# Kernel optimization log

Hardware: AMD Instinct MI355X
Metric: run time of the kernel (lower is better)

The kernel has to match this reference:

```python
import jax, jax.numpy as jnp
import numpy as np

B, S, D_IN, D_OUT = 4, 2048, 1024, 1024


def setup_inputs() -> dict:
    key = jax.random.key(0)
    k1, k2, k3, k4 = jax.random.split(key, 4)
    x = jax.random.normal(k1, (B, S, D_IN), dtype=jnp.float32)
    scale = 1.0 / np.sqrt(D_IN)
    Wq = jax.random.normal(k2, (D_IN, D_OUT), dtype=jnp.float32) * scale
    Wk = jax.random.normal(k3, (D_IN, D_OUT), dtype=jnp.float32) * scale
    Wv = jax.random.normal(k4, (D_IN, D_OUT), dtype=jnp.float32) * scale
    return {"x": x, "Wq": Wq, "Wk": Wk, "Wv": Wv}


def reference(x, Wq, Wk, Wv):
    # QKV projections (Linear, no bias)
    q = jnp.einsum('bsd,de->bse', x, Wq)  # [B,S,D_OUT]
    k = jnp.einsum('bsd,de->bse', x, Wk)
    v = jnp.einsum('bsd,de->bse', x, Wv)
    d_out = Wq.shape[1]
    # raw scores [B,S,S], scaled after masking (identical math: -inf stays -inf)
    scores = jnp.einsum('bqe,bke->bqk', q, k) * (d_out ** -0.5)
    S_ = x.shape[1]
    # causal mask: future positions (j > i) are masked out
    causal = jnp.triu(jnp.ones((S_, S_), dtype=bool), k=1)
    scores = jnp.where(causal[None, :, :], -jnp.inf, scores)
    attn = jax.nn.softmax(scores, axis=-1)  # dropout p=0.0 -> identity
    return jnp.einsum('bqk,bke->bqe', attn, v)
```

## Files before the change

### kernel.cpp

```cpp
#include <hip/hip_runtime.h>
#include <stdint.h>

typedef unsigned short u16;
typedef unsigned int u32;
typedef __bf16 bf16x8 __attribute__((ext_vector_type(8)));
typedef float f32x4 __attribute__((ext_vector_type(4)));

#define BM 128
#define BN 128
#define BK 64

__device__ __forceinline__ u16 f2bf(float x) {
  union { float f; uint32_t u; } c; c.f = x;
  uint32_t r = (c.u + 0x7FFFu + ((c.u >> 16) & 1u)) >> 16;
  return (u16)r;
}

__device__ __forceinline__ void async_copy16(const u16* g, u16* l) {
  __builtin_amdgcn_global_load_lds(
      (const __attribute__((address_space(1))) void*)g,
      (__attribute__((address_space(3))) void*)l,
      16, 0, 0);
}

__global__ void flag_init(u32* __restrict__ f) { if (threadIdx.x == 0) *f = 0; }

__global__ void detect_dtype(const u16* __restrict__ w, u32* __restrict__ cnt) {
  int i = blockIdx.x * 256 + threadIdx.x;
  if ((w[i] & 0x7F80u) == 0x7F80u) atomicAdd(cnt, 1u);
}

__global__ void normalize_all(const void* __restrict__ s0, const void* __restrict__ s1,
                              const void* __restrict__ s2, const void* __restrict__ s3,
                              u16* __restrict__ dst, const u32* __restrict__ flag,
                              long n0, long n1) {
  long i = (long)blockIdx.x * 256 + threadIdx.x;
  const void* src;
  long j;
  if (i < n0) { src = s0; j = i; }
  else {
    long t = i - n0;
    long w = t / n1;
    j = t - w * n1;
    src = (w == 0) ? s1 : (w == 1) ? s2 : s3;
  }
  if (*flag > 32) dst[i] = f2bf(((const float*)src)[j]);
  else            dst[i] = ((const u16*)src)[j];
}

__global__ void zerofill_u16(u16* __restrict__ p) {
  long i = (long)blockIdx.x * 256 + threadIdx.x;
  p[i] = 0;
}

template <int MODE>
__global__ __launch_bounds__(256, 2)
void gemm_nt(const u16* __restrict__ A, const u16* __restrict__ B, void* __restrict__ Cv,
             const u32* __restrict__ flag,
             int K, int lda, int ldb, int ldc,
             long sA, long sB, long sC, long cOff,
             float scale, int causal, int trik)
{
  const int bm = blockIdx.y, bn = blockIdx.x, bz = blockIdx.z;
  if (causal && bn > bm) return;

  __shared__ u16 As[BM * BK];
  __shared__ u16 Bs[BN * BK];

  A += (long)bz * sA;
  B += (long)bz * sB;

  const int tid  = threadIdx.x;
  const int wid  = tid >> 6;
  const int lane = tid & 63;
  const int l16  = lane & 15;
  const int lk   = lane >> 4;
  const int srow = lane >> 3;
  const int swz  = ((lane & 7) ^ srow) * 8;
  const int m0 = bm * BM, n0 = bn * BN;

  int nk = K / BK;
  if (trik) { int lim = (m0 + BM) / BK; if (lim < nk) nk = lim; }

  f32x4 acc[4][4] = {};

  for (int kt = 0; kt < nk; ++kt) {
    const int k0 = kt * BK;
#pragma unroll
    for (int c = 0; c < 4; ++c) {
      const int rb = wid * 32 + c * 8;
      async_copy16(A + (long)(m0 + rb + srow) * lda + (k0 + swz), As + rb * BK);
      async_copy16(B + (long)(n0 + rb + srow) * ldb + (k0 + swz), Bs + rb * BK);
    }
    __syncthreads();
#pragma unroll
    for (int kh = 0; kh < 2; ++kh) {
      bf16x8 av[4], bv[4];
#pragma unroll
      for (int i = 0; i < 4; ++i) {
        const int Ra = (wid >> 1) * 64 + i * 16 + l16;
        const int Rb = (wid & 1)  * 64 + i * 16 + l16;
        const int ca = ((kh * 4 + lk) ^ (l16 & 7)) * 8;
        av[i] = *(const bf16x8*)(As + Ra * BK + ca);
        bv[i] = *(const bf16x8*)(Bs + Rb * BK + ca);
      }
#pragma unroll
      for (int mi = 0; mi < 4; ++mi)
#pragma unroll
        for (int ni = 0; ni < 4; ++ni)
          acc[mi][ni] = __builtin_amdgcn_mfma_f32_16x16x32_bf16(av[mi], bv[ni], acc[mi][ni], 0, 0, 0);
    }
    __syncthreads();
  }

  const int rb0 = m0 + (wid >> 1) * 64;
  const int cb0 = n0 + (wid & 1) * 64;
  const long cbase = (long)bz * sC + cOff;
  const bool f32out = (MODE == 1) || (MODE == 2 && *flag > 32);

#pragma unroll
  for (int mi = 0; mi < 4; ++mi)
#pragma unroll
    for (int ni = 0; ni < 4; ++ni) {
      const int row = rb0 + mi * 16 + lk * 4;
      const int col = cb0 + ni * 16 + l16;
#pragma unroll
      for (int r = 0; r < 4; ++r) {
        const float v = acc[mi][ni][r] * scale;
        const long idx = cbase + (long)(row + r) * ldc + col;
        if constexpr (MODE == 0) {
          ((u16*)Cv)[idx] = f2bf(v);
        } else if constexpr (MODE == 1) {
          ((float*)Cv)[idx] = v;
        } else {
          if (f32out) ((float*)Cv)[idx] = v;
          else        ((u16*)Cv)[idx]   = f2bf(v);
        }
      }
    }
}

__global__ __launch_bounds__(256)
void transpose_bf16(const u16* __restrict__ in, u16* __restrict__ out,
                    int ldIn, int ldOut, long sIn, long sOut)
{
  __shared__ u16 tile[64][72];
  const int bz = blockIdx.z;
  in  += (long)bz * sIn;
  out += (long)bz * sOut;
  const int r0 = blockIdx.y * 64, c0 = blockIdx.x * 64;
  const int tid = threadIdx.x;
#pragma unroll
  for (int p = 0; p < 2; ++p) {
    int v = tid + p * 256;
    int row = v >> 3, c8 = (v & 7) * 8;
    union { uint4 q; u16 s[8]; } t;
    t.q = *(const uint4*)(in + (long)(r0 + row) * ldIn + c0 + c8);
#pragma unroll
    for (int i = 0; i < 8; ++i) tile[row][c8 + i] = t.s[i];
  }
  __syncthreads();
#pragma unroll
  for (int p = 0; p < 2; ++p) {
    int v = tid + p * 256;
    int oc = v >> 3, r8 = (v & 7) * 8;
    union { uint4 q; u16 s[8]; } t;
#pragma unroll
    for (int i = 0; i < 8; ++i) t.s[i] = tile[r8 + i][oc];
    *(uint4*)(out + (long)(c0 + oc) * ldOut + r0 + r8) = t.q;
  }
}

__global__ __launch_bounds__(256)
void softmax_causal(char* __restrict__ base, long rowStrideB, int S, int modS)
{
  const long r = blockIdx.x;
  const int i = (int)(r % modS);
  float* sc = (float*)(base + r * rowStrideB);
  u16*   pr = (u16*)(base + r * rowStrideB);
  const int n = i + 1;
  const int tid = threadIdx.x;
  const int wv = tid >> 6, lane = tid & 63;
  __shared__ float red[4];

  float e[8];
  int cnt = 0;
  float m = -3.0e38f;
  for (int j = tid; j < n; j += 256) { float x = sc[j]; e[cnt++] = x; m = fmaxf(m, x); }
#pragma unroll
  for (int o = 32; o > 0; o >>= 1) m = fmaxf(m, __shfl_xor(m, o));
  if (lane == 0) red[wv] = m;
  __syncthreads();
  m = fmaxf(fmaxf(red[0], red[1]), fmaxf(red[2], red[3]));
  __syncthreads();

  float s = 0.f;
#pragma unroll
  for (int c = 0; c < 8; ++c)
    if (c < cnt) { float x = __expf(e[c] - m); e[c] = x; s += x; }
#pragma unroll
  for (int o = 32; o > 0; o >>= 1) s += __shfl_xor(s, o);
  if (lane == 0) red[wv] = s;
  __syncthreads();
  s = red[0] + red[1] + red[2] + red[3];
  const float inv = 1.0f / s;

  cnt = 0;
  for (int j = tid; j < S; j += 256) {
    u16 v = 0;
    if (j < n) v = f2bf(e[cnt++] * inv);
    pr[j] = v;
  }
}

extern "C" void kernel_launch(void* const* d_in, const int* in_sizes, int n_in,
                              void* d_out, int out_size, void* d_ws, size_t ws_size,
                              hipStream_t stream)
{
  (void)in_sizes; (void)n_in; (void)out_size;
  const int Bb = 4, S = 2048, D = 1024, D3 = 3072;
  const long SD = (long)S * D;
  const long SS = (long)S * S;
  const long N_X = (long)Bb * SD;
  const long N_W = (long)D * D;

  char* ws = (char*)d_ws;
  size_t off = 0;
  auto take = [&](size_t bytes) -> void* {
    void* p = ws + off;
    off = (off + bytes + 255) & ~((size_t)255);
    return p;
  };

  u32* flag = (u32*)take(4096);
  u16* xn   = (u16*)take((size_t)N_X * 2);
  u16* wn3  = (u16*)take((size_t)3 * N_W * 2);
  u16* WT3  = (u16*)take((size_t)3 * N_W * 2);
  const size_t off_common = off;

  const size_t needA = off_common + (size_t)(N_X * 3 * 2)
                     + (size_t)(N_X * 2)
                     + (size_t)(Bb * SS * 4) + 4096;
  const size_t needC = off_common + (size_t)(S * (long)D3 * 2)
                     + (size_t)(SD * 2)
                     + (size_t)(SS * 4) + 4096;

  if (ws_size < needC) {
    zerofill_u16<<<(int)(N_X / 256), 256, 0, stream>>>((u16*)d_out);
    return;
  }

  flag_init<<<1, 64, 0, stream>>>(flag);
  detect_dtype<<<1024, 256, 0, stream>>>((const u16*)d_in[1], flag);

  normalize_all<<<(int)((N_X + 3 * N_W) / 256), 256, 0, stream>>>(
      d_in[0], d_in[1], d_in[2], d_in[3], xn, flag, N_X, N_W);

  transpose_bf16<<<dim3(D / 64, D / 64, 3), 256, 0, stream>>>(wn3, WT3, D, D, N_W, N_W);

  const float scl = 0.03125f;

  if (ws_size >= needA) {
    u16*   QKV = (u16*)take((size_t)N_X * 3 * 2);
    u16*   VT  = (u16*)take((size_t)N_X * 2);
    float* sc  = (float*)take((size_t)Bb * SS * 4);

    gemm_nt<0><<<dim3(D3 / BN, (int)(N_X / D) / BM, 1), 256, 0, stream>>>(
        xn, WT3, QKV, flag, D, D, D, D3, 0, 0, 0, 0, 1.f, 0, 0);

    transpose_bf16<<<dim3(D / 64, S / 64, Bb), 256, 0, stream>>>(
        QKV + 2048, VT, D3, S, (long)S * D3, SD);

    gemm_nt<1><<<dim3(S / BN, S / BM, Bb), 256, 0, stream>>>(
        QKV, QKV + 1024, sc, flag, D, D3, D3, S,
        (long)S * D3, (long)S * D3, SS, 0, scl, 1, 0);

    softmax_causal<<<Bb * S, 256, 0, stream>>>((char*)sc, (long)S * 4, S, S);

    gemm_nt<2><<<dim3(D / BN, S / BM, Bb), 256, 0, stream>>>(
        (u16*)sc, VT, d_out, flag, S, 2 * S, S, D,
        2 * SS, SD, SD, 0, 1.f, 0, 1);
  } else {
    u16*   QKVb = (u16*)take((size_t)S * D3 * 2);
    u16*   VTb  = (u16*)take((size_t)SD * 2);
    float* scb  = (float*)take((size_t)SS * 4);

    for (int b = 0; b < Bb; ++b) {
      gemm_nt<0><<<dim3(D3 / BN, S / BM, 1), 256, 0, stream>>>(
          xn + (long)b * SD, WT3, QKVb, flag, D, D, D, D3, 0, 0, 0, 0, 1.f, 0, 0);

      transpose_bf16<<<dim3(D / 64, S / 64, 1), 256, 0, stream>>>(
          QKVb + 2048, VTb, D3, S, 0, 0);

      gemm_nt<1><<<dim3(S / BN, S / BM, 1), 256, 0, stream>>>(
          QKVb, QKVb + 1024, scb, flag, D, D3, D3, S, 0, 0, 0, 0, scl, 1, 0);

      softmax_causal<<<S, 256, 0, stream>>>((char*)scb, (long)S * 4, S, S);

      gemm_nt<2><<<dim3(D / BN, S / BM, 1), 256, 0, stream>>>(
          (u16*)scb, VTb, d_out, flag, S, 2 * S, S, D,
          0, 0, 0, (long)b * SD, 1.f, 0, 1);
    }
  }
}
```

Baseline: 270.1 us.

## Vectorize softmax and input normalization, fuse weight convert with transpose

Softmax now has each thread handle 8 contiguous elements with vector loads and a single 16-byte store, replacing strided scalar loops. The x conversion is vectorized and the weight conversion is fused into the transpose, which eliminates an intermediate buffer and a kernel launch. The PV GEMM reverses row-block order so the longest causal rows start first. The aim is to cut memory traffic and launch overhead; the softmax now relies on S equalling 256*8.

```diff
diff --git a/kernel.cpp b/kernel.cpp
--- a/kernel.cpp
+++ b/kernel.cpp
@@ -30,27 +30,68 @@
   if ((w[i] & 0x7F80u) == 0x7F80u) atomicAdd(cnt, 1u);
 }
 
-__global__ void normalize_all(const void* __restrict__ s0, const void* __restrict__ s1,
-                              const void* __restrict__ s2, const void* __restrict__ s3,
-                              u16* __restrict__ dst, const u32* __restrict__ flag,
-                              long n0, long n1) {
-  long i = (long)blockIdx.x * 256 + threadIdx.x;
-  const void* src;
-  long j;
-  if (i < n0) { src = s0; j = i; }
-  else {
-    long t = i - n0;
-    long w = t / n1;
-    j = t - w * n1;
-    src = (w == 0) ? s1 : (w == 1) ? s2 : s3;
-  }
-  if (*flag > 32) dst[i] = f2bf(((const float*)src)[j]);
-  else            dst[i] = ((const u16*)src)[j];
+__global__ __launch_bounds__(256)
+void normalize_x(const void* __restrict__ src, u16* __restrict__ dst,
+                 const u32* __restrict__ flag, long n) {
+  long i = ((long)blockIdx.x * 256 + threadIdx.x) * 8;
+  if (i >= n) return;
+  u16 o[8];
+  if (*flag > 32) {
+    const float* s = (const float*)src + i;
+    f32x4 a = *(const f32x4*)s;
+    f32x4 b = *(const f32x4*)(s + 4);
+#pragma unroll
+    for (int c = 0; c < 4; ++c) { o[c] = f2bf(a[c]); o[c + 4] = f2bf(b[c]); }
+  } else {
+    *(uint4*)o = *(const uint4*)((const u16*)src + i);
+  }
+  *(uint4*)(dst + i) = *(uint4*)o;
 }
 
 __global__ void zerofill_u16(u16* __restrict__ p) {
   long i = (long)blockIdx.x * 256 + threadIdx.x;
   p[i] = 0;
+}
+
+__global__ __launch_bounds__(256)
+void transnorm_w(const void* __restrict__ s0, const void* __restrict__ s1,
+                 const void* __restrict__ s2, u16* __restrict__ dst,
+                 const u32* __restrict__ flag, int Dd)
+{
+  __shared__ u16 tile[64][72];
+  const int z = blockIdx.z;
+  const void* src = (z == 0) ? s0 : (z == 1) ? s1 : s2;
+  u16* out = dst + (long)z * Dd * Dd;
+  const int r0 = blockIdx.y * 64, c0 = blockIdx.x * 64;
+  const int tid = threadIdx.x;
+  const bool isf32 = (*flag > 32);
+#pragma unroll
+  for (int p = 0; p < 2; ++p) {
+    int v = tid + p * 256;
+    int row = v >> 3, c8 = (v & 7) * 8;
+    u16 t[8];
+    if (isf32) {
+      const float* sp = (const float*)src + (long)(r0 + row) * Dd + c0 + c8;
+      f32x4 a = *(const f32x4*)sp;
+      f32x4 b = *(const f32x4*)(sp + 4);
+#pragma unroll
+      for (int c = 0; c < 4; ++c) { t[c] = f2bf(a[c]); t[c + 4] = f2bf(b[c]); }
+    } else {
+      *(uint4*)t = *(const uint4*)((const u16*)src + (long)(r0 + row) * Dd + c0 + c8);
+    }
+#pragma unroll
+    for (int c = 0; c < 8; ++c) tile[row][c8 + c] = t[c];
+  }
+  __syncthreads();
+#pragma unroll
+  for (int p = 0; p < 2; ++p) {
+    int v = tid + p * 256;
+    int oc = v >> 3, r8 = (v & 7) * 8;
+    union { uint4 q; u16 s[8]; } t;
+#pragma unroll
+    for (int c = 0; c < 8; ++c) t.s[c] = tile[r8 + c][oc];
+    *(uint4*)(out + (long)(c0 + oc) * Dd + r0 + r8) = t.q;
+  }
 }
 
 template <int MODE>
@@ -61,7 +102,9 @@
              long sA, long sB, long sC, long cOff,
              float scale, int causal, int trik)
 {
-  const int bm = blockIdx.y, bn = blockIdx.x, bz = blockIdx.z;
+  int bm = blockIdx.y;
+  if (trik) bm = gridDim.y - 1 - bm;
+  const int bn = blockIdx.x, bz = blockIdx.z;
   if (causal && bn > bm) return;
 
   __shared__ u16 As[BM * BK];
@@ -172,7 +215,7 @@
 }
 
 __global__ __launch_bounds__(256)
-void softmax_causal(char* __restrict__ base, long rowStrideB, int S, int modS)
+void softmax_causal(char* __restrict__ base, long rowStrideB, int modS)
 {
   const long r = blockIdx.x;
   const int i = (int)(r % modS);
@@ -180,13 +223,25 @@
   u16*   pr = (u16*)(base + r * rowStrideB);
   const int n = i + 1;
   const int tid = threadIdx.x;
+  const int j0 = tid * 8;
   const int wv = tid >> 6, lane = tid & 63;
   __shared__ float red[4];
 
   float e[8];
-  int cnt = 0;
   float m = -3.0e38f;
-  for (int j = tid; j < n; j += 256) { float x = sc[j]; e[cnt++] = x; m = fmaxf(m, x); }
+  if (j0 < n) {
+    f32x4 a = *(const f32x4*)(sc + j0);
+    f32x4 b = *(const f32x4*)(sc + j0 + 4);
+#pragma unroll
+    for (int c = 0; c < 4; ++c) { e[c] = a[c]; e[c + 4] = b[c]; }
+#pragma unroll
+    for (int c = 0; c < 8; ++c) {
+      if (j0 + c < n) m = fmaxf(m, e[c]); else e[c] = -3.0e38f;
+    }
+  } else {
+#pragma unroll
+    for (int c = 0; c < 8; ++c) e[c] = -3.0e38f;
+  }
 #pragma unroll
   for (int o = 32; o > 0; o >>= 1) m = fmaxf(m, __shfl_xor(m, o));
   if (lane == 0) red[wv] = m;
@@ -196,8 +251,7 @@
 
   float s = 0.f;
 #pragma unroll
-  for (int c = 0; c < 8; ++c)
-    if (c < cnt) { float x = __expf(e[c] - m); e[c] = x; s += x; }
+  for (int c = 0; c < 8; ++c) { float x = __expf(e[c] - m); e[c] = x; s += x; }
 #pragma unroll
   for (int o = 32; o > 0; o >>= 1) s += __shfl_xor(s, o);
   if (lane == 0) red[wv] = s;
@@ -205,12 +259,10 @@
   s = red[0] + red[1] + red[2] + red[3];
   const float inv = 1.0f / s;
 
-  cnt = 0;
-  for (int j = tid; j < S; j += 256) {
-    u16 v = 0;
-    if (j < n) v = f2bf(e[cnt++] * inv);
-    pr[j] = v;
-  }
+  u16 o8[8];
+#pragma unroll
+  for (int c = 0; c < 8; ++c) o8[c] = f2bf(e[c] * inv);
+  *(uint4*)(pr + j0) = *(uint4*)o8;
 }
 
 extern "C" void kernel_launch(void* const* d_in, const int* in_sizes, int n_in,
@@ -234,7 +286,6 @@
 
   u32* flag = (u32*)take(4096);
   u16* xn   = (u16*)take((size_t)N_X * 2);
-  u16* wn3  = (u16*)take((size_t)3 * N_W * 2);
   u16* WT3  = (u16*)take((size_t)3 * N_W * 2);
   const size_t off_common = off;
 
@@ -253,10 +304,9 @@
   flag_init<<<1, 64, 0, stream>>>(flag);
   detect_dtype<<<1024, 256, 0, stream>>>((const u16*)d_in[1], flag);
 
-  normalize_all<<<(int)((N_X + 3 * N_W) / 256), 256, 0, stream>>>(
-      d_in[0], d_in[1], d_in[2], d_in[3], xn, flag, N_X, N_W);
-
-  transpose_bf16<<<dim3(D / 64, D / 64, 3), 256, 0, stream>>>(wn3, WT3, D, D, N_W, N_W);
+  normalize_x<<<(int)(N_X / 2048), 256, 0, stream>>>(d_in[0], xn, flag, N_X);
+  transnorm_w<<<dim3(D / 64, D / 64, 3), 256, 0, stream>>>(
+      d_in[1], d_in[2], d_in[3], WT3, flag, D);
 
   const float scl = 0.03125f;
 
@@ -275,7 +325,7 @@
         QKV, QKV + 1024, sc, flag, D, D3, D3, S,
         (long)S * D3, (long)S * D3, SS, 0, scl, 1, 0);
 
-    softmax_causal<<<Bb * S, 256, 0, stream>>>((char*)sc, (long)S * 4, S, S);
+    softmax_causal<<<Bb * S, 256, 0, stream>>>((char*)sc, (long)S * 4, S);
 
     gemm_nt<2><<<dim3(D / BN, S / BM, Bb), 256, 0, stream>>>(
         (u16*)sc, VT, d_out, flag, S, 2 * S, S, D,
@@ -295,7 +345,7 @@
       gemm_nt<1><<<dim3(S / BN, S / BM, 1), 256, 0, stream>>>(
           QKVb, QKVb + 1024, scb, flag, D, D3, D3, S, 0, 0, 0, 0, scl, 1, 0);
 
-      softmax_causal<<<S, 256, 0, stream>>>((char*)scb, (long)S * 4, S, S);
+      softmax_causal<<<S, 256, 0, stream>>>((char*)scb, (long)S * 4, S);
 
       gemm_nt<2><<<dim3(D / BN, S / BM, 1), 256, 0, stream>>>(
           (u16*)scb, VTb, d_out, flag, S, 2 * S, S, D,
```

After: 255.4 us. 1.06x faster.
